# Kernel tuning notes

Hardware: AMD Instinct MI355X
Metric: run time of the kernel (lower is better)

## Reference

```python
import jax, jax.numpy as jnp
import numpy as np

B, S, D_IN, D_OUT, H = 2, 2048, 1024, 1024, 16
HD = D_OUT // H  # 64


def setup_inputs() -> dict:
    key = jax.random.key(0)
    ks = jax.random.split(key, 6)
    s = 0.02
    return {
        "x": jax.random.normal(ks[0], (B, S, D_IN), dtype=jnp.float32),
        "W_q": jax.random.normal(ks[1], (D_IN, D_OUT), dtype=jnp.float32) * s,
        "W_k": jax.random.normal(ks[2], (D_IN, D_OUT), dtype=jnp.float32) * s,
        "W_v": jax.random.normal(ks[3], (D_IN, D_OUT), dtype=jnp.float32) * s,
        "W_o": jax.random.normal(ks[4], (D_OUT, D_OUT), dtype=jnp.float32) * s,
        "b_o": jax.random.normal(ks[5], (D_OUT,), dtype=jnp.float32) * s,
    }


def reference(x, W_q, W_k, W_v, W_o, b_o):
    b, n, _ = x.shape
    # project and split heads: [b, h, n, hd]
    q = (x @ W_q).reshape(b, n, H, HD).transpose(0, 2, 1, 3)
    k = (x @ W_k).reshape(b, n, H, HD).transpose(0, 2, 1, 3)
    v = (x @ W_v).reshape(b, n, H, HD).transpose(0, 2, 1, 3)
    scores = jnp.einsum("bhqd,bhkd->bhqk", q, k) / jnp.sqrt(jnp.float32(HD))
    causal = jnp.tril(jnp.ones((n, n), dtype=bool))
    scores = jnp.where(causal, scores, -jnp.inf)
    attn = jax.nn.softmax(scores, axis=-1)  # dropout p=0.0 -> identity
    ctx = jnp.einsum("bhqk,bhkd->bhqd", attn, v)
    ctx = ctx.transpose(0, 2, 1, 3).reshape(b, n, D_OUT)
    return ctx @ W_o + b_o
```

## Files before the change

### kernel.cpp

```cpp
#include <hip/hip_runtime.h>

#define B_    2
#define S_    2048
#define DIN   1024
#define DOUT  1024
#define H_    16
#define HD_   64
#define M_    (B_ * S_)

typedef __bf16 bf16x8 __attribute__((ext_vector_type(8)));
typedef float  f32x4  __attribute__((ext_vector_type(4)));

__device__ __forceinline__ f32x4 MFMA(bf16x8 a, bf16x8 b, f32x4 c) {
    return __builtin_amdgcn_mfma_f32_16x16x32_bf16(a, b, c, 0, 0, 0);
}

__device__ __forceinline__ unsigned short f2b(float f) {
    union { float f; unsigned int u; } v; v.f = f;
    unsigned int u = v.u;
    return (unsigned short)((u + 0x7fffu + ((u >> 16) & 1u)) >> 16);
}

__device__ __forceinline__ unsigned pack2(float a, float b) {
    union { __bf16 h[2]; unsigned u; } cv;
    cv.h[0] = (__bf16)a; cv.h[1] = (__bf16)b;
    return cv.u;
}

#define GLDS(gp, lp) __builtin_amdgcn_global_load_lds( \
    (const __attribute__((address_space(1))) void*)(gp), \
    (__attribute__((address_space(3))) void*)(lp), 16, 0, 0)

#define QSCALE 0.1803368801111204f

__global__ __launch_bounds__(256) void k_cvt_all(const float* __restrict__ x,
                                                 const float* __restrict__ Wq,
                                                 const float* __restrict__ Wk,
                                                 const float* __restrict__ Wv,
                                                 const float* __restrict__ Wo,
                                                 unsigned short* __restrict__ xb,
                                                 unsigned short* __restrict__ WqkvT,
                                                 unsigned short* __restrict__ WoT) {
    __shared__ float tile[32][33];
    int bid = blockIdx.x;
    if (bid < 4096) {
        int i = (bid * 256 + threadIdx.x) * 4;
        float4 v = *reinterpret_cast<const float4*>(x + i);
        ushort4 o;
        o.x = f2b(v.x); o.y = f2b(v.y); o.z = f2b(v.z); o.w = f2b(v.w);
        *reinterpret_cast<ushort4*>(xb + i) = o;
        return;
    }
    int wb = bid - 4096;
    int w = wb >> 10;
    int t = wb & 1023;
    const float* src = (w == 0) ? Wq : (w == 1) ? Wk : (w == 2) ? Wv : Wo;
    unsigned short* dst = (w < 3) ? WqkvT + (size_t)w * 1024 * DIN : WoT;
    int n0 = (t & 31) * 32, k0 = (t >> 5) * 32;
    int tx = threadIdx.x & 31, ty = threadIdx.x >> 5;
    for (int i = 0; i < 4; i++)
        tile[ty + i * 8][tx] = src[(size_t)(k0 + ty + i * 8) * DOUT + n0 + tx];
    __syncthreads();
    for (int i = 0; i < 4; i++)
        dst[(size_t)(n0 + ty + i * 8) * DIN + k0 + tx] = f2b(tile[tx][ty + i * 8]);
}

__global__ __launch_bounds__(256) void k_trV(const unsigned short* __restrict__ V,
                                             unsigned short* __restrict__ Vt) {
    __shared__ unsigned short tile[64][72];
    int st = blockIdx.x, bh = blockIdx.y;
    int b = bh >> 4, h = bh & 15;
    int t = threadIdx.x;
    int r = t >> 2, c = (t & 3) << 4;
    const unsigned short* src = V + (size_t)(b * S_ + st * 64 + r) * DOUT + h * HD_ + c;
    *reinterpret_cast<int4*>(&tile[r][c])     = *reinterpret_cast<const int4*>(src);
    *reinterpret_cast<int4*>(&tile[r][c + 8]) = *reinterpret_cast<const int4*>(src + 8);
    __syncthreads();
    unsigned short o[16];
    for (int j = 0; j < 16; j++) o[j] = tile[c + j][r];
    unsigned short* dst = Vt + (size_t)(bh * 64 + r) * S_ + st * 64 + c;
    *reinterpret_cast<int4*>(dst)     = *reinterpret_cast<int4*>(&o[0]);
    *reinterpret_cast<int4*>(dst + 8) = *reinterpret_cast<int4*>(&o[8]);
}

template <int OUT_MODE>
__global__ __launch_bounds__(256) void k_gemm(const unsigned short* __restrict__ A,
                                              const unsigned short* __restrict__ Bt,
                                              unsigned short* __restrict__ Cq,
                                              unsigned short* __restrict__ Ck,
                                              unsigned short* __restrict__ Cv,
                                              float* __restrict__ Cf,
                                              const float* __restrict__ bias,
                                              int M, int N, int K, int nbx) {
    __shared__ __align__(16) unsigned short As[128 * 64];
    __shared__ __align__(16) unsigned short Bs[128 * 64];

    int nwg = gridDim.x;
    int chunkw = nwg >> 3;
    int bid = blockIdx.x;
    int nid = (bid & 7) * chunkw + (bid >> 3);
    int by = nid / nbx, bx = nid - by * nbx;
    int m0 = by * 128, n0 = bx * 128;

    int tid = threadIdx.x;
    int wid = tid >> 6, lane = tid & 63;
    int wm = wid >> 1, wn = wid & 1;
    int lr = lane & 15, lg = lane >> 4;

    f32x4 acc[4][4] = {};

    int srow = lane >> 3;
    int scol = ((lane & 7) ^ srow) * 8;
    int rsw  = lr & 7;

    for (int k0 = 0; k0 < K; k0 += 64) {
#pragma unroll
        for (int c = 0; c < 4; c++) {
            int chunk = wid * 4 + c;
            int row = chunk * 8 + srow;
            GLDS(A  + (size_t)(m0 + row) * K + k0 + scol, (char*)As + chunk * 1024);
            GLDS(Bt + (size_t)(n0 + row) * K + k0 + scol, (char*)Bs + chunk * 1024);
        }
        __syncthreads();

#pragma unroll
        for (int kk = 0; kk < 2; kk++) {
            bf16x8 af[4], bf[4];
#pragma unroll
            for (int mi = 0; mi < 4; mi++)
                af[mi] = *reinterpret_cast<const bf16x8*>(
                    &As[(wm * 64 + mi * 16 + lr) * 64 + (((kk * 4 + lg) ^ rsw) * 8)]);
#pragma unroll
            for (int ni = 0; ni < 4; ni++)
                bf[ni] = *reinterpret_cast<const bf16x8*>(
                    &Bs[(wn * 64 + ni * 16 + lr) * 64 + (((kk * 4 + lg) ^ rsw) * 8)]);
#pragma unroll
            for (int mi = 0; mi < 4; mi++)
#pragma unroll
                for (int ni = 0; ni < 4; ni++)
                    acc[mi][ni] = MFMA(af[mi], bf[ni], acc[mi][ni]);
        }
        __syncthreads();
    }

    for (int mi = 0; mi < 4; mi++)
        for (int ni = 0; ni < 4; ni++)
            for (int i = 0; i < 4; i++) {
                int row = m0 + wm * 64 + mi * 16 + lg * 4 + i;
                int col = n0 + wn * 64 + ni * 16 + lr;
                float v = acc[mi][ni][i];
                if (OUT_MODE == 2) {
                    Cf[(size_t)row * N + col] = v + bias[col];
                } else {
                    if (col < 1024)       Cq[(size_t)row * 1024 + col] = f2b(v * QSCALE);
                    else if (col < 2048)  Ck[(size_t)row * 1024 + (col - 1024)] = f2b(v);
                    else                  Cv[(size_t)row * 1024 + (col - 2048)] = f2b(v);
                }
            }
}

__device__ __forceinline__ void sm_store(f32x4 (&s)[8], unsigned* __restrict__ pl32,
                                         float& l, int qg, int kv0, bool diag,
                                         int lr, int lg) {
    if (diag) {
#pragma unroll
        for (int nf = 0; nf < 8; nf++)
#pragma unroll
            for (int i = 0; i < 4; i++)
                if (kv0 + nf * 16 + lg * 4 + i > qg) s[nf][i] = -2000.0f;
    }
    f32x4 acc = {};
#pragma unroll
    for (int nf = 0; nf < 8; nf++) {
        f32x4 pv;
#pragma unroll
        for (int i = 0; i < 4; i++) pv[i] = exp2f(s[nf][i]);
        acc += pv;
        unsigned w0 = pack2(pv[0], pv[1]);
        unsigned w1 = pack2(pv[2], pv[3]);
        int unit = (nf * 2 + (lg >> 1)) ^ (lr & 7);
        uint2 wd; wd.x = w0; wd.y = w1;
        *reinterpret_cast<uint2*>(&pl32[lr * 64 + unit * 4 + (lg & 1) * 2]) = wd;
    }
    l += (acc[0] + acc[1]) + (acc[2] + acc[3]);
}

template <bool WITHA>
__device__ __forceinline__ void tile_body(const unsigned short* __restrict__ Kt,
                                          const unsigned short* __restrict__ Vl,
                                          unsigned* __restrict__ pl32,
                                          bf16x8 qB0, bf16x8 qB1, bf16x8 qA0, bf16x8 qA1,
                                          f32x4 (&oB)[4], f32x4 (&oA)[4],
                                          float& lB, float& lA,
                                          int qgB, int qgA, int kv0, bool dgB, bool dgA,
                                          int lr, int lg, int rxor) {
    f32x4 sB[8], sA[8];
#pragma unroll
    for (int nf = 0; nf < 8; nf++) { sB[nf] = {}; if (WITHA) sA[nf] = {}; }
    __builtin_amdgcn_s_setprio(1);
#pragma unroll
    for (int nf = 0; nf < 8; nf++) {
#pragma unroll
        for (int kk = 0; kk < 2; kk++) {
            bf16x8 kf = *reinterpret_cast<const bf16x8*>(
                &Kt[(nf * 16 + lr) * 64 + (((kk * 64 + lg * 16) ^ rxor) >> 1)]);
            sB[nf] = MFMA(kf, kk ? qB1 : qB0, sB[nf]);
            if (WITHA) sA[nf] = MFMA(kf, kk ? qA1 : qA0, sA[nf]);
        }
    }
    __builtin_amdgcn_s_setprio(0);

    sm_store(sB, pl32, lB, qgB, kv0, dgB, lr, lg);
    bf16x8 pfB[4], pfA[4];
#pragma unroll
    for (int kvb = 0; kvb < 4; kvb++)
        pfB[kvb] = *reinterpret_cast<const bf16x8*>(
            &pl32[lr * 64 + (((kvb * 4 + lg) ^ (lr & 7)) * 4)]);
    if (WITHA) {
        sm_store(sA, pl32, lA, qgA, kv0, dgA, lr, lg);
#pragma unroll
        for (int kvb = 0; kvb < 4; kvb++)
            pfA[kvb] = *reinterpret_cast<const bf16x8*>(
                &pl32[lr * 64 + (((kvb * 4 + lg) ^ (lr & 7)) * 4)]);
    }

    __builtin_amdgcn_s_setprio(1);
#pragma unroll
    for (int nd = 0; nd < 4; nd++)
#pragma unroll
        for (int kk = 0; kk < 4; kk++) {
            bf16x8 vf = *reinterpret_cast<const bf16x8*>(
                &Vl[(nd * 16 + lr) * 128 + (((kk * 64 + lg * 16) ^ rxor) >> 1)]);
            oB[nd] = MFMA(pfB[kk], vf, oB[nd]);
            if (WITHA) oA[nd] = MFMA(pfA[kk], vf, oA[nd]);
        }
    __builtin_amdgcn_s_setprio(0);
}

__global__ __launch_bounds__(256, 2) void k_attn(const unsigned short* __restrict__ Q,
                                                 const unsigned short* __restrict__ Kg,
                                                 const unsigned short* __restrict__ Vt,
                                                 unsigned short* __restrict__ ctx) {
    int p = blockIdx.x;
    int bh = blockIdx.y;
    int b = bh >> 4, h = bh & 15;
    int tid = threadIdx.x, wid = tid >> 6, lane = tid & 63;
    int lr = lane & 15, lg = lane >> 4;
    int qtA = p, qtB = 31 - p;
    int q0A = qtA * 64 + wid * 16;
    int q0B = qtB * 64 + wid * 16;

    __shared__ __align__(16) unsigned short Ks[2][128 * 64];
    __shared__ __align__(16) unsigned short Vs[2][64 * 128];
    __shared__ __align__(16) unsigned p_lds32[4][16 * 64];
    unsigned* pl32 = p_lds32[wid];

    const unsigned short* Qp = Q  + (size_t)b * S_ * DOUT + (size_t)h * HD_;
    const unsigned short* Kp = Kg + (size_t)b * S_ * DOUT + (size_t)h * HD_;
    const unsigned short* Vp = Vt + (size_t)(b * H_ + h) * HD_ * S_;

    bf16x8 qfA0 = *reinterpret_cast<const bf16x8*>(&Qp[(size_t)(q0A + lr) * DOUT + lg * 8]);
    bf16x8 qfA1 = *reinterpret_cast<const bf16x8*>(&Qp[(size_t)(q0A + lr) * DOUT + 32 + lg * 8]);
    bf16x8 qfB0 = *reinterpret_cast<const bf16x8*>(&Qp[(size_t)(q0B + lr) * DOUT + lg * 8]);
    bf16x8 qfB1 = *reinterpret_cast<const bf16x8*>(&Qp[(size_t)(q0B + lr) * DOUT + 32 + lg * 8]);
    asm volatile("" : "+v"(qfA0), "+v"(qfA1), "+v"(qfB0), "+v"(qfB1));

#define STAGE_KV(buf, t)                                                           \
    {                                                                              \
        int kv0_ = (t) * 128;                                                      \
        for (int c = 0; c < 4; c++) {                                              \
            int kc = wid * 4 + c;                                                  \
            int krow = kc * 8 + (lane >> 3);                                       \
            int kcol = ((lane & 7) ^ (lane >> 3)) * 8;                             \
            GLDS(Kp + (size_t)(kv0_ + krow) * DOUT + kcol,                         \
                 (char*)&Ks[buf][0] + kc * 1024);                                  \
            int vrow = kc * 4 + (lane >> 4);                                       \
            int vcol = ((lane & 15) ^ (vrow & 7)) * 8;                             \
            GLDS(Vp + (size_t)vrow * S_ + kv0_ + vcol,                             \
                 (char*)&Vs[buf][0] + kc * 1024);                                  \
        }                                                                          \
    }

    STAGE_KV(0, 0)

    f32x4 oA[4] = {}, oB[4] = {};
    float lA = 0.f, lB = 0.f;

    int diagA = (qtA * 64 + 63) >> 7;
    int diagB = (qtB * 64 + 63) >> 7;
    int ntile = diagB + 1;
    int rxor = (lr & 7) << 4;
    int qgA = q0A + lr, qgB = q0B + lr;

    for (int t = 0; t < ntile; t++) {
        int cur = t & 1;
        if (t + 1 < ntile) {
            STAGE_KV(cur ^ 1, t + 1)
            asm volatile("s_waitcnt vmcnt(8)" ::: "memory");
        } else {
            asm volatile("s_waitcnt vmcnt(0)" ::: "memory");
        }
        __builtin_amdgcn_s_barrier();

        int kv0 = t * 128;
        const unsigned short* Kt = Ks[cur];
        const unsigned short* Vl = Vs[cur];

        if (t <= diagA)
            tile_body<true>(Kt, Vl, pl32, qfB0, qfB1, qfA0, qfA1, oB, oA,
                            lB, lA, qgB, qgA, kv0, t == diagB, t == diagA,
                            lr, lg, rxor);
        else
            tile_body<false>(Kt, Vl, pl32, qfB0, qfB1, qfA0, qfA1, oB, oA,
                             lB, lA, qgB, qgA, kv0, t == diagB, false,
                             lr, lg, rxor);

        __builtin_amdgcn_s_barrier();
    }

    lB += __shfl_xor(lB, 16, 64);
    lB += __shfl_xor(lB, 32, 64);
    lA += __shfl_xor(lA, 16, 64);
    lA += __shfl_xor(lA, 32, 64);

#pragma unroll
    for (int i = 0; i < 4; i++) {
        float liB = __shfl(lB, lg * 4 + i, 16);
        float liA = __shfl(lA, lg * 4 + i, 16);
        float rB = __builtin_amdgcn_rcpf(liB);
        float rA = __builtin_amdgcn_rcpf(liA);
#pragma unroll
        for (int nd = 0; nd < 4; nd++) {
            ((__bf16*)ctx)[((size_t)b * S_ + q0B + lg * 4 + i) * DOUT + h * HD_ + nd * 16 + lr] =
                (__bf16)(oB[nd][i] * rB);
            ((__bf16*)ctx)[((size_t)b * S_ + q0A + lg * 4 + i) * DOUT + h * HD_ + nd * 16 + lr] =
                (__bf16)(oA[nd][i] * rA);
        }
    }
#undef STAGE_KV
}

extern "C" void kernel_launch(void* const* d_in, const int* in_sizes, int n_in,
                              void* d_out, int out_size, void* d_ws, size_t ws_size,
                              hipStream_t stream) {
    const float* x  = (const float*)d_in[0];
    const float* Wq = (const float*)d_in[1];
    const float* Wk = (const float*)d_in[2];
    const float* Wv = (const float*)d_in[3];
    const float* Wo = (const float*)d_in[4];
    const float* bo = (const float*)d_in[5];
    float* out = (float*)d_out;
    char* ws = (char*)d_ws;
    const size_t MB = 1u << 20;

    unsigned short* xb    = (unsigned short*)(ws);
    unsigned short* Vtb   = (unsigned short*)(ws);
    unsigned short* WqkvT = (unsigned short*)(ws + 8 * MB);
    unsigned short* WoT   = (unsigned short*)(ws + 14 * MB);
    unsigned short* Qb    = (unsigned short*)(ws + 16 * MB);
    unsigned short* Kb    = (unsigned short*)(ws + 24 * MB);
    unsigned short* Vb    = (unsigned short*)(ws + 32 * MB);
    unsigned short* ctx   = Vb;

    (void)in_sizes; (void)n_in; (void)out_size; (void)ws_size;

    k_cvt_all<<<8192, 256, 0, stream>>>(x, Wq, Wk, Wv, Wo, xb, WqkvT, WoT);

    k_gemm<0><<<768, 256, 0, stream>>>(xb, WqkvT, Qb, Kb, Vb, nullptr, nullptr,
                                       M_, 3072, DIN, 24);

    dim3 gt(S_ / 64, B_ * H_);
    k_trV<<<gt, 256, 0, stream>>>(Vb, Vtb);

    dim3 ga(16, B_ * H_);
    k_attn<<<ga, 256, 0, stream>>>(Qb, Kb, Vtb, ctx);

    k_gemm<2><<<256, 256, 0, stream>>>(ctx, WoT, nullptr, nullptr, nullptr,
                                       out, bo, M_, DOUT, DOUT, 8);
}
```

Before: 122.2 us.

## Split paired query tiles across 8 waves with 64-wide KV tiles

The attention kernel now uses 512 threads per block. Waves 0-3 handle the late query tile and waves 4-7 handle the early one, where before each wave held both. The KV tile shrinks from 128 to 64 keys, which halves shared memory per stage and lowers per-wave register pressure, so more waves can be resident. In exchange, waves on the short tile sit idle at barriers for the rest of the loop, and there are twice as many barrier iterations per block.

```diff
diff --git a/kernel.cpp b/kernel.cpp
--- a/kernel.cpp
+++ b/kernel.cpp
@@ -159,85 +159,7 @@
             }
 }
 
-__device__ __forceinline__ void sm_store(f32x4 (&s)[8], unsigned* __restrict__ pl32,
-                                         float& l, int qg, int kv0, bool diag,
-                                         int lr, int lg) {
-    if (diag) {
-#pragma unroll
-        for (int nf = 0; nf < 8; nf++)
-#pragma unroll
-            for (int i = 0; i < 4; i++)
-                if (kv0 + nf * 16 + lg * 4 + i > qg) s[nf][i] = -2000.0f;
-    }
-    f32x4 acc = {};
-#pragma unroll
-    for (int nf = 0; nf < 8; nf++) {
-        f32x4 pv;
-#pragma unroll
-        for (int i = 0; i < 4; i++) pv[i] = exp2f(s[nf][i]);
-        acc += pv;
-        unsigned w0 = pack2(pv[0], pv[1]);
-        unsigned w1 = pack2(pv[2], pv[3]);
-        int unit = (nf * 2 + (lg >> 1)) ^ (lr & 7);
-        uint2 wd; wd.x = w0; wd.y = w1;
-        *reinterpret_cast<uint2*>(&pl32[lr * 64 + unit * 4 + (lg & 1) * 2]) = wd;
-    }
-    l += (acc[0] + acc[1]) + (acc[2] + acc[3]);
-}
-
-template <bool WITHA>
-__device__ __forceinline__ void tile_body(const unsigned short* __restrict__ Kt,
-                                          const unsigned short* __restrict__ Vl,
-                                          unsigned* __restrict__ pl32,
-                                          bf16x8 qB0, bf16x8 qB1, bf16x8 qA0, bf16x8 qA1,
-                                          f32x4 (&oB)[4], f32x4 (&oA)[4],
-                                          float& lB, float& lA,
-                                          int qgB, int qgA, int kv0, bool dgB, bool dgA,
-                                          int lr, int lg, int rxor) {
-    f32x4 sB[8], sA[8];
-#pragma unroll
-    for (int nf = 0; nf < 8; nf++) { sB[nf] = {}; if (WITHA) sA[nf] = {}; }
-    __builtin_amdgcn_s_setprio(1);
-#pragma unroll
-    for (int nf = 0; nf < 8; nf++) {
-#pragma unroll
-        for (int kk = 0; kk < 2; kk++) {
-            bf16x8 kf = *reinterpret_cast<const bf16x8*>(
-                &Kt[(nf * 16 + lr) * 64 + (((kk * 64 + lg * 16) ^ rxor) >> 1)]);
-            sB[nf] = MFMA(kf, kk ? qB1 : qB0, sB[nf]);
-            if (WITHA) sA[nf] = MFMA(kf, kk ? qA1 : qA0, sA[nf]);
-        }
-    }
-    __builtin_amdgcn_s_setprio(0);
-
-    sm_store(sB, pl32, lB, qgB, kv0, dgB, lr, lg);
-    bf16x8 pfB[4], pfA[4];
-#pragma unroll
-    for (int kvb = 0; kvb < 4; kvb++)
-        pfB[kvb] = *reinterpret_cast<const bf16x8*>(
-            &pl32[lr * 64 + (((kvb * 4 + lg) ^ (lr & 7)) * 4)]);
-    if (WITHA) {
-        sm_store(sA, pl32, lA, qgA, kv0, dgA, lr, lg);
-#pragma unroll
-        for (int kvb = 0; kvb < 4; kvb++)
-            pfA[kvb] = *reinterpret_cast<const bf16x8*>(
-                &pl32[lr * 64 + (((kvb * 4 + lg) ^ (lr & 7)) * 4)]);
-    }
-
-    __builtin_amdgcn_s_setprio(1);
-#pragma unroll
-    for (int nd = 0; nd < 4; nd++)
-#pragma unroll
-        for (int kk = 0; kk < 4; kk++) {
-            bf16x8 vf = *reinterpret_cast<const bf16x8*>(
-                &Vl[(nd * 16 + lr) * 128 + (((kk * 64 + lg * 16) ^ rxor) >> 1)]);
-            oB[nd] = MFMA(pfB[kk], vf, oB[nd]);
-            if (WITHA) oA[nd] = MFMA(pfA[kk], vf, oA[nd]);
-        }
-    __builtin_amdgcn_s_setprio(0);
-}
-
-__global__ __launch_bounds__(256, 2) void k_attn(const unsigned short* __restrict__ Q,
+__global__ __launch_bounds__(512, 4) void k_attn(const unsigned short* __restrict__ Q,
                                                  const unsigned short* __restrict__ Kg,
                                                  const unsigned short* __restrict__ Vt,
                                                  unsigned short* __restrict__ ctx) {
@@ -246,96 +168,127 @@
     int b = bh >> 4, h = bh & 15;
     int tid = threadIdx.x, wid = tid >> 6, lane = tid & 63;
     int lr = lane & 15, lg = lane >> 4;
-    int qtA = p, qtB = 31 - p;
-    int q0A = qtA * 64 + wid * 16;
-    int q0B = qtB * 64 + wid * 16;
-
-    __shared__ __align__(16) unsigned short Ks[2][128 * 64];
-    __shared__ __align__(16) unsigned short Vs[2][64 * 128];
-    __shared__ __align__(16) unsigned p_lds32[4][16 * 64];
+    int qtB = 31 - p;
+    int qt = (wid < 4) ? qtB : p;
+    int q0 = qt * 64 + (wid & 3) * 16;
+
+    __shared__ __align__(16) unsigned short Ks[2][64 * 64];
+    __shared__ __align__(16) unsigned short Vs[2][64 * 64];
+    __shared__ __align__(16) unsigned p_lds32[8][16 * 32];
     unsigned* pl32 = p_lds32[wid];
 
     const unsigned short* Qp = Q  + (size_t)b * S_ * DOUT + (size_t)h * HD_;
     const unsigned short* Kp = Kg + (size_t)b * S_ * DOUT + (size_t)h * HD_;
     const unsigned short* Vp = Vt + (size_t)(b * H_ + h) * HD_ * S_;
 
-    bf16x8 qfA0 = *reinterpret_cast<const bf16x8*>(&Qp[(size_t)(q0A + lr) * DOUT + lg * 8]);
-    bf16x8 qfA1 = *reinterpret_cast<const bf16x8*>(&Qp[(size_t)(q0A + lr) * DOUT + 32 + lg * 8]);
-    bf16x8 qfB0 = *reinterpret_cast<const bf16x8*>(&Qp[(size_t)(q0B + lr) * DOUT + lg * 8]);
-    bf16x8 qfB1 = *reinterpret_cast<const bf16x8*>(&Qp[(size_t)(q0B + lr) * DOUT + 32 + lg * 8]);
-    asm volatile("" : "+v"(qfA0), "+v"(qfA1), "+v"(qfB0), "+v"(qfB1));
+    bf16x8 qf0 = *reinterpret_cast<const bf16x8*>(&Qp[(size_t)(q0 + lr) * DOUT + lg * 8]);
+    bf16x8 qf1 = *reinterpret_cast<const bf16x8*>(&Qp[(size_t)(q0 + lr) * DOUT + 32 + lg * 8]);
+    asm volatile("" : "+v"(qf0), "+v"(qf1));
+
+    int srow = lane >> 3;
+    int scol = ((lane & 7) ^ srow) * 8;
 
 #define STAGE_KV(buf, t)                                                           \
     {                                                                              \
-        int kv0_ = (t) * 128;                                                      \
-        for (int c = 0; c < 4; c++) {                                              \
-            int kc = wid * 4 + c;                                                  \
-            int krow = kc * 8 + (lane >> 3);                                       \
-            int kcol = ((lane & 7) ^ (lane >> 3)) * 8;                             \
-            GLDS(Kp + (size_t)(kv0_ + krow) * DOUT + kcol,                         \
-                 (char*)&Ks[buf][0] + kc * 1024);                                  \
-            int vrow = kc * 4 + (lane >> 4);                                       \
-            int vcol = ((lane & 15) ^ (vrow & 7)) * 8;                             \
-            GLDS(Vp + (size_t)vrow * S_ + kv0_ + vcol,                             \
-                 (char*)&Vs[buf][0] + kc * 1024);                                  \
-        }                                                                          \
+        int kv0_ = (t) * 64;                                                       \
+        int krow = wid * 8 + srow;                                                 \
+        GLDS(Kp + (size_t)(kv0_ + krow) * DOUT + scol,                             \
+             (char*)&Ks[buf][0] + wid * 1024);                                     \
+        GLDS(Vp + (size_t)krow * S_ + kv0_ + scol,                                 \
+             (char*)&Vs[buf][0] + wid * 1024);                                     \
     }
 
     STAGE_KV(0, 0)
 
-    f32x4 oA[4] = {}, oB[4] = {};
-    float lA = 0.f, lB = 0.f;
-
-    int diagA = (qtA * 64 + 63) >> 7;
-    int diagB = (qtB * 64 + 63) >> 7;
-    int ntile = diagB + 1;
+    f32x4 o[4] = {};
+    float l = 0.f;
+
+    int ntile = qtB + 1;
     int rxor = (lr & 7) << 4;
-    int qgA = q0A + lr, qgB = q0B + lr;
+    int qg = q0 + lr;
 
     for (int t = 0; t < ntile; t++) {
         int cur = t & 1;
         if (t + 1 < ntile) {
             STAGE_KV(cur ^ 1, t + 1)
-            asm volatile("s_waitcnt vmcnt(8)" ::: "memory");
+            asm volatile("s_waitcnt vmcnt(2)" ::: "memory");
         } else {
             asm volatile("s_waitcnt vmcnt(0)" ::: "memory");
         }
         __builtin_amdgcn_s_barrier();
 
-        int kv0 = t * 128;
-        const unsigned short* Kt = Ks[cur];
-        const unsigned short* Vl = Vs[cur];
-
-        if (t <= diagA)
-            tile_body<true>(Kt, Vl, pl32, qfB0, qfB1, qfA0, qfA1, oB, oA,
-                            lB, lA, qgB, qgA, kv0, t == diagB, t == diagA,
-                            lr, lg, rxor);
-        else
-            tile_body<false>(Kt, Vl, pl32, qfB0, qfB1, qfA0, qfA1, oB, oA,
-                             lB, lA, qgB, qgA, kv0, t == diagB, false,
-                             lr, lg, rxor);
+        if (t <= qt) {
+            const unsigned short* Kt = Ks[cur];
+            const unsigned short* Vl = Vs[cur];
+            int kv0 = t * 64;
+
+            f32x4 s[4] = {};
+            __builtin_amdgcn_s_setprio(1);
+#pragma unroll
+            for (int nf = 0; nf < 4; nf++)
+#pragma unroll
+                for (int kk = 0; kk < 2; kk++) {
+                    bf16x8 kf = *reinterpret_cast<const bf16x8*>(
+                        &Kt[(nf * 16 + lr) * 64 + (((kk * 64 + lg * 16) ^ rxor) >> 1)]);
+                    s[nf] = MFMA(kf, kk ? qf1 : qf0, s[nf]);
+                }
+            __builtin_amdgcn_s_setprio(0);
+
+            if (t == qt) {
+#pragma unroll
+                for (int nf = 0; nf < 4; nf++)
+#pragma unroll
+                    for (int i = 0; i < 4; i++)
+                        if (kv0 + nf * 16 + lg * 4 + i > qg) s[nf][i] = -2000.0f;
+            }
+
+            f32x4 acc = {};
+#pragma unroll
+            for (int nf = 0; nf < 4; nf++) {
+                f32x4 pv;
+#pragma unroll
+                for (int i = 0; i < 4; i++) pv[i] = exp2f(s[nf][i]);
+                acc += pv;
+                unsigned w0 = pack2(pv[0], pv[1]);
+                unsigned w1 = pack2(pv[2], pv[3]);
+                int unit = (nf * 2 + (lg >> 1)) ^ (lr & 7);
+                uint2 wd; wd.x = w0; wd.y = w1;
+                *reinterpret_cast<uint2*>(&pl32[lr * 32 + unit * 4 + (lg & 1) * 2]) = wd;
+            }
+            l += (acc[0] + acc[1]) + (acc[2] + acc[3]);
+
+            bf16x8 pf[2];
+#pragma unroll
+            for (int kvb = 0; kvb < 2; kvb++)
+                pf[kvb] = *reinterpret_cast<const bf16x8*>(
+                    &pl32[lr * 32 + (((kvb * 4 + lg) ^ (lr & 7)) * 4)]);
+
+            __builtin_amdgcn_s_setprio(1);
+#pragma unroll
+            for (int nd = 0; nd < 4; nd++)
+#pragma unroll
+                for (int kk = 0; kk < 2; kk++) {
+                    bf16x8 vf = *reinterpret_cast<const bf16x8*>(
+                        &Vl[(nd * 16 + lr) * 64 + (((kk * 64 + lg * 16) ^ rxor) >> 1)]);
+                    o[nd] = MFMA(pf[kk], vf, o[nd]);
+                }
+            __builtin_amdgcn_s_setprio(0);
+        }
 
         __builtin_amdgcn_s_barrier();
     }
 
-    lB += __shfl_xor(lB, 16, 64);
-    lB += __shfl_xor(lB, 32, 64);
-    lA += __shfl_xor(lA, 16, 64);
-    lA += __shfl_xor(lA, 32, 64);
+    l += __shfl_xor(l, 16, 64);
+    l += __shfl_xor(l, 32, 64);
 
 #pragma unroll
     for (int i = 0; i < 4; i++) {
-        float liB = __shfl(lB, lg * 4 + i, 16);
-        float liA = __shfl(lA, lg * 4 + i, 16);
-        float rB = __builtin_amdgcn_rcpf(liB);
-        float rA = __builtin_amdgcn_rcpf(liA);
-#pragma unroll
-        for (int nd = 0; nd < 4; nd++) {
-            ((__bf16*)ctx)[((size_t)b * S_ + q0B + lg * 4 + i) * DOUT + h * HD_ + nd * 16 + lr] =
-                (__bf16)(oB[nd][i] * rB);
-            ((__bf16*)ctx)[((size_t)b * S_ + q0A + lg * 4 + i) * DOUT + h * HD_ + nd * 16 + lr] =
-                (__bf16)(oA[nd][i] * rA);
-        }
+        float li = __shfl(l, lg * 4 + i, 16);
+        float r = __builtin_amdgcn_rcpf(li);
+#pragma unroll
+        for (int nd = 0; nd < 4; nd++)
+            ((__bf16*)ctx)[((size_t)b * S_ + q0 + lg * 4 + i) * DOUT + h * HD_ + nd * 16 + lr] =
+                (__bf16)(o[nd][i] * r);
     }
 #undef STAGE_KV
 }
@@ -373,7 +326,7 @@
     k_trV<<<gt, 256, 0, stream>>>(Vb, Vtb);
 
     dim3 ga(16, B_ * H_);
-    k_attn<<<ga, 256, 0, stream>>>(Qb, Kb, Vtb, ctx);
+    k_attn<<<ga, 512, 0, stream>>>(Qb, Kb, Vtb, ctx);
 
     k_gemm<2><<<256, 256, 0, stream>>>(ctx, WoT, nullptr, nullptr, nullptr,
                                        out, bo, M_, DOUT, DOUT, 8);
```

Result: no change. 120.8 us (-1.2%).
